# Performance work log

Measured on AMD Instinct MI355X. Metric: run time of the kernel, lower is better.

The kernel has to match this reference:

```python
import math
import jax, jax.numpy as jnp
import numpy as np

B, CIN, COUT, K, T, S = 16, 512, 512, 3, 2048, 128


def setup_inputs() -> dict:
    key = jax.random.key(0)
    k1, k2, k3, k4 = jax.random.split(key, 4)
    x = jax.random.normal(k1, (B, CIN, T), dtype=jnp.float32)
    c_trg = jax.random.normal(k2, (B, S), dtype=jnp.float32)
    style_w = jax.random.normal(k3, (CIN, S), dtype=jnp.float32)  # EqualLinear weight (lr_mul=1)
    style_b = jnp.ones((CIN,), dtype=jnp.float32)  # bias_init=1
    conv_w = jax.random.normal(k4, (1, COUT, CIN, K), dtype=jnp.float32)
    return {"x": x, "c_trg": c_trg, "style_w": style_w, "style_b": style_b, "conv_w": conv_w}


def reference(x, c_trg, style_w, style_b, conv_w):
    b, cin, t = x.shape
    cout, k = conv_w.shape[1], conv_w.shape[3]
    lin_scale = 1.0 / math.sqrt(style_w.shape[1])  # EqualLinear scale, lr_mul=1
    # original forward calls style_linear twice -> s and b are the SAME value
    s = c_trg @ (style_w * lin_scale).T + style_b            # [B, Cin]
    s = s[:, None, :, None]                                   # [B, 1, Cin, 1]
    conv_scale = 1.0 / math.sqrt(cin * k ** 2)
    w = conv_scale * (conv_w * s + s)                         # [B, Cout, Cin, K]
    demod = jax.lax.rsqrt(jnp.sum(w * w, axis=(2, 3)) + 1e-8)  # [B, Cout]
    demod_mean = jnp.mean(w.reshape(b, cout, -1), axis=2)      # [B, Cout]
    w = (w - demod_mean[:, :, None, None]) * demod[:, :, None, None]
    pad = k // 2

    def conv1(xi, wi):  # xi [Cin, T], wi [Cout, Cin, K]
        return jax.lax.conv_general_dilated(
            xi[None], wi, window_strides=(1,), padding=[(pad, pad)],
            dimension_numbers=("NCH", "OIH", "NCH"))[0]

    out = jax.vmap(conv1)(x, w)  # [B, Cout, T]
    return out
```

## Files before the change

### kernel.cpp

```cpp
#include <hip/hip_runtime.h>
#include <hip/hip_bf16.h>
#include <stdint.h>

#define B_    16
#define CIN_  512
#define COUT_ 512
#define K_    3
#define T_    2048
#define S_    128
#define TP_   2064
#define CXP_  2050

#define LIN_SCALE  0.08838834764831845f
#define CONV_SCALE 0.014731391274719739f

typedef unsigned short u16;
typedef short s16x8 __attribute__((ext_vector_type(8)));
typedef float f32x4 __attribute__((ext_vector_type(4)));
typedef u16 u16x8 __attribute__((ext_vector_type(8)));

__device__ __forceinline__ u16 bf16r(float f) {
    uint32_t u = __float_as_uint(f);
    return (u16)((u + 0x7FFFu + ((u >> 16) & 1u)) >> 16);
}

#define GLDS16(gsrc, ldst) \
    __builtin_amdgcn_global_load_lds((__attribute__((address_space(1))) void*)(gsrc), \
                                     (__attribute__((address_space(3))) void*)(ldst), 16, 0, 0)

__global__ void k_style(const float* __restrict__ c_trg,
                        const float* __restrict__ style_w,
                        const float* __restrict__ style_b,
                        float* __restrict__ s_out) {
    int idx = blockIdx.x * 256 + threadIdx.x;
    int b = idx >> 9, i = idx & 511;
    const float4* c4 = reinterpret_cast<const float4*>(c_trg + b * S_);
    const float4* w4 = reinterpret_cast<const float4*>(style_w + (size_t)i * S_);
    float acc = 0.f;
#pragma unroll
    for (int j = 0; j < S_ / 4; ++j) {
        float4 a = c4[j], w = w4[j];
        acc += a.x * w.x + a.y * w.y + a.z * w.z + a.w * w.w;
    }
    s_out[idx] = acc * LIN_SCALE + style_b[i];
}

__global__ void k_wsum(const float* __restrict__ conv_w,
                       float* __restrict__ W1, float* __restrict__ W2) {
    int idx = blockIdx.x * 256 + threadIdx.x;
    const float* wr = conv_w + (size_t)idx * 3;
    float a0 = wr[0] + 1.f, a1 = wr[1] + 1.f, a2 = wr[2] + 1.f;
    W1[idx] = a0 + a1 + a2;
    W2[idx] = a0 * a0 + a1 * a1 + a2 * a2;
}

__global__ void k_stats2(const float* __restrict__ s,
                         const float* __restrict__ W1, const float* __restrict__ W2,
                         float* __restrict__ alpha, float* __restrict__ beta) {
    int bo = blockIdx.x;
    int b = bo >> 9, o = bo & 511;
    const float* sb = s + b * CIN_;
    const float* w1 = W1 + (size_t)o * CIN_;
    const float* w2 = W2 + (size_t)o * CIN_;
    int l = threadIdx.x;
    float sum = 0.f, sq = 0.f;
#pragma unroll
    for (int r = 0; r < 8; ++r) {
        float sv = sb[l + r * 64];
        sum += sv * w1[l + r * 64];
        sq  += sv * sv * w2[l + r * 64];
    }
#pragma unroll
    for (int off = 32; off; off >>= 1) { sum += __shfl_down(sum, off); sq += __shfl_down(sq, off); }
    if (l == 0) {
        float mean  = CONV_SCALE * sum * (1.0f / (CIN_ * K_));
        float demod = rsqrtf(CONV_SCALE * CONV_SCALE * sq + 1e-8f);
        alpha[bo] = demod * CONV_SCALE;
        beta[bo]  = demod * mean;
    }
}

__global__ void k_prep_w(const float* __restrict__ conv_w, u16* __restrict__ wpk) {
    int idx = blockIdx.x * 256 + threadIdx.x;
    int j    = idx & 7;
    int lane = (idx >> 3) & 63;
    int grp  = (idx >> 9) & 7;
    int rest = idx >> 12;
    int tap  = rest % 3;
    int so   = rest / 3;
    int step = so & 15, ob = so >> 4;
    int o = ob * 128 + grp * 16 + (lane & 15);
    int i = step * 32 + (lane >> 4) * 8 + j;
    wpk[idx] = bf16r(conv_w[((size_t)o * CIN_ + i) * 3 + tap]);
}

__global__ void k_ytrans(const float* __restrict__ x, const float* __restrict__ s,
                         u16* __restrict__ ybf,
                         float* __restrict__ cxp, float* __restrict__ cyp) {
    int t = blockIdx.x * 256 + threadIdx.x;
    int oct = blockIdx.y, b = blockIdx.z;
    const float* xb = x + ((size_t)(b * CIN_ + oct * 8)) * T_ + t;
    const float* sb = s + b * CIN_ + oct * 8;
    float ax = 0.f, ay = 0.f;
    u16x8 pv;
#pragma unroll
    for (int j = 0; j < 8; ++j) {
        float xv = xb[(size_t)j * T_];
        float yv = sb[j] * xv;
        ax += xv; ay += yv;
        pv[j] = bf16r(yv);
    }
    *(u16x8*)(ybf + (((size_t)(b * 64 + oct)) * TP_ + t + 8) * 8) = pv;
    atomicAdd(&cxp[b * CXP_ + t + 1], ax);
    atomicAdd(&cyp[b * CXP_ + t + 1], ay);
    if (blockIdx.x == 0 && threadIdx.x < 8) {
        u16x8 z = {0, 0, 0, 0, 0, 0, 0, 0};
        *(u16x8*)(ybf + (((size_t)(b * 64 + oct)) * TP_ + threadIdx.x) * 8) = z;
    }
    if (blockIdx.x == 7 && threadIdx.x >= 248) {
        u16x8 z = {0, 0, 0, 0, 0, 0, 0, 0};
        *(u16x8*)(ybf + (((size_t)(b * 64 + oct)) * TP_ + 2056 + (threadIdx.x - 248)) * 8) = z;
    }
}

__global__ __launch_bounds__(256) void k_conv(
    const u16* __restrict__ wpk, const u16* __restrict__ ybf,
    const float* __restrict__ alpha, const float* __restrict__ beta,
    const float* __restrict__ cxp, const float* __restrict__ cyp,
    float* __restrict__ out) {

    __shared__ __align__(16) char smem[33792];

    const int tid  = threadIdx.x;
    const int lane = tid & 63;
    const int w    = tid >> 6;
    const int wr   = w >> 1, wc = w & 1;
    const int t0   = blockIdx.x * 128;
    const int ob   = blockIdx.y;
    const int b    = blockIdx.z;

    f32x4 acc[4][4] = {};

    const char* wsrc  = (const char*)wpk + (size_t)(ob * 16) * 24576 + (w * 6) * 1024 + lane * 16;
    const char* ybase = (const char*)ybf + ((size_t)b * 64) * (TP_ * 16);

    const int as_lane = wr * 4096 + lane * 16;
    const int xs_lane = 24576 + (lane >> 4) * 2304 + ((lane & 15) + 7) * 16 + wc * 1024;

    for (int step = 0; step < 16; ++step) {
        __syncthreads();
#pragma unroll
        for (int r = 0; r < 6; ++r)
            GLDS16(wsrc + (size_t)step * 24576 + r * 1024, smem + (w * 6 + r) * 1024);
#pragma unroll
        for (int rb = w; rb < 9; rb += 4) {
            int c  = rb * 64 + lane;
            int g  = c / 144;
            int rr = c - g * 144;
            GLDS16(ybase + ((size_t)((step * 4 + g) * TP_) + t0 + rr) * 16,
                   smem + 24576 + rb * 1024);
        }
        __syncthreads();

#pragma unroll
        for (int tap = 0; tap < 3; ++tap) {
            s16x8 af[4], bq[4];
#pragma unroll
            for (int m = 0; m < 4; ++m)
                af[m] = *(const s16x8*)(smem + tap * 8192 + as_lane + m * 1024);
#pragma unroll
            for (int n = 0; n < 4; ++n)
                bq[n] = *(const s16x8*)(smem + xs_lane + tap * 16 + n * 256);
#pragma unroll
            for (int m = 0; m < 4; ++m)
#pragma unroll
                for (int n = 0; n < 4; ++n)
                    acc[m][n] = __builtin_amdgcn_mfma_f32_16x16x32_bf16(af[m], bq[n], acc[m][n], 0, 0, 0);
        }
    }

    const int lr = lane >> 4, lc = lane & 15;
    const int o0 = ob * 128 + wr * 64;
    const int tw = t0 + wc * 64;
    const float* al  = alpha + b * COUT_ + o0;
    const float* be  = beta  + b * COUT_ + o0;
    const float* cxb = cxp + b * CXP_;
    const float* cyb = cyp + b * CXP_;
    float* op = out + ((size_t)(b * COUT_ + o0)) * T_;

#pragma unroll
    for (int n = 0; n < 4; ++n) {
        int t = tw + n * 16 + lc;
        float cx3 = cxb[t] + cxb[t + 1] + cxb[t + 2];
        float cy3 = cyb[t] + cyb[t + 1] + cyb[t + 2];
#pragma unroll
        for (int m = 0; m < 4; ++m)
#pragma unroll
            for (int q = 0; q < 4; ++q) {
                int o = m * 16 + lr * 4 + q;
                op[(size_t)o * T_ + t] = al[o] * (acc[m][n][q] + cy3) - be[o] * cx3;
            }
    }
}

extern "C" void kernel_launch(void* const* d_in, const int* in_sizes, int n_in,
                              void* d_out, int out_size, void* d_ws, size_t ws_size,
                              hipStream_t stream) {
    const float* x       = (const float*)d_in[0];
    const float* c_trg   = (const float*)d_in[1];
    const float* style_w = (const float*)d_in[2];
    const float* style_b = (const float*)d_in[3];
    const float* conv_w  = (const float*)d_in[4];
    float* out = (float*)d_out;
    float* ws  = (float*)d_ws;

    float* s_buf = ws;
    float* alpha = ws + 8192;
    float* beta  = ws + 16384;
    float* cxp   = ws + 24576;
    float* cyp   = ws + 57376;
    float* W1    = ws + 90176;
    float* W2    = ws + 352320;
    u16*   wpk   = (u16*)(ws + 614464);
    u16*   ybf   = (u16*)(ws + 1007680);

    hipMemsetAsync(cxp, 0, (size_t)2 * CXP_ * B_ * sizeof(float), stream);

    k_style <<<dim3((B_ * CIN_) / 256), 256, 0, stream>>>(c_trg, style_w, style_b, s_buf);
    k_wsum  <<<dim3((COUT_ * CIN_) / 256), 256, 0, stream>>>(conv_w, W1, W2);
    k_prep_w<<<dim3((COUT_ * CIN_ * K_) / 256), 256, 0, stream>>>(conv_w, wpk);
    k_stats2<<<dim3(B_ * COUT_), 64, 0, stream>>>(s_buf, W1, W2, alpha, beta);
    k_ytrans<<<dim3(T_ / 256, CIN_ / 8, B_), 256, 0, stream>>>(x, s_buf, ybf, cxp, cyp);
    k_conv  <<<dim3(T_ / 128, COUT_ / 128, B_), 256, 0, stream>>>(wpk, ybf, alpha, beta, cxp, cyp, out);
}
```

Before: 226.2 us.

## Double-buffer conv LDS loads, remap blocks, replace atomic column sums with reduction

```diff
diff --git a/kernel.cpp b/kernel.cpp
--- a/kernel.cpp
+++ b/kernel.cpp
@@ -96,7 +96,7 @@
 
 __global__ void k_ytrans(const float* __restrict__ x, const float* __restrict__ s,
                          u16* __restrict__ ybf,
-                         float* __restrict__ cxp, float* __restrict__ cyp) {
+                         float* __restrict__ cxpart, float* __restrict__ cypart) {
     int t = blockIdx.x * 256 + threadIdx.x;
     int oct = blockIdx.y, b = blockIdx.z;
     const float* xb = x + ((size_t)(b * CIN_ + oct * 8)) * T_ + t;
@@ -111,8 +111,8 @@
         pv[j] = bf16r(yv);
     }
     *(u16x8*)(ybf + (((size_t)(b * 64 + oct)) * TP_ + t + 8) * 8) = pv;
-    atomicAdd(&cxp[b * CXP_ + t + 1], ax);
-    atomicAdd(&cyp[b * CXP_ + t + 1], ay);
+    cxpart[((size_t)(b * 64 + oct)) * T_ + t] = ax;
+    cypart[((size_t)(b * 64 + oct)) * T_ + t] = ay;
     if (blockIdx.x == 0 && threadIdx.x < 8) {
         u16x8 z = {0, 0, 0, 0, 0, 0, 0, 0};
         *(u16x8*)(ybf + (((size_t)(b * 64 + oct)) * TP_ + threadIdx.x) * 8) = z;
@@ -121,6 +121,22 @@
         u16x8 z = {0, 0, 0, 0, 0, 0, 0, 0};
         *(u16x8*)(ybf + (((size_t)(b * 64 + oct)) * TP_ + 2056 + (threadIdx.x - 248)) * 8) = z;
     }
+}
+
+__global__ void k_colred(const float* __restrict__ cxpart, const float* __restrict__ cypart,
+                         float* __restrict__ cxp, float* __restrict__ cyp) {
+    int t = blockIdx.x * 256 + threadIdx.x;
+    int b = blockIdx.y;
+    float sx = 0.f, sy = 0.f;
+#pragma unroll 8
+    for (int oct = 0; oct < 64; ++oct) {
+        sx += cxpart[((size_t)(b * 64 + oct)) * T_ + t];
+        sy += cypart[((size_t)(b * 64 + oct)) * T_ + t];
+    }
+    cxp[b * CXP_ + t + 1] = sx;
+    cyp[b * CXP_ + t + 1] = sy;
+    if (t == 0)        { cxp[b * CXP_] = 0.f;        cyp[b * CXP_] = 0.f; }
+    if (t == T_ - 1)   { cxp[b * CXP_ + T_ + 1] = 0.f; cyp[b * CXP_ + T_ + 1] = 0.f; }
 }
 
 __global__ __launch_bounds__(256) void k_conv(
@@ -129,15 +145,18 @@
     const float* __restrict__ cxp, const float* __restrict__ cyp,
     float* __restrict__ out) {
 
-    __shared__ __align__(16) char smem[33792];
+    __shared__ __align__(16) char smem[2 * 33792];
 
     const int tid  = threadIdx.x;
     const int lane = tid & 63;
     const int w    = tid >> 6;
     const int wr   = w >> 1, wc = w & 1;
-    const int t0   = blockIdx.x * 128;
-    const int ob   = blockIdx.y;
-    const int b    = blockIdx.z;
+
+    const int bid = blockIdx.x;
+    const int wg  = (bid & 7) * 128 + (bid >> 3);
+    const int b   = wg >> 6;
+    const int ob  = (wg >> 4) & 3;
+    const int t0  = (wg & 15) * 128;
 
     f32x4 acc[4][4] = {};
 
@@ -147,37 +166,49 @@
     const int as_lane = wr * 4096 + lane * 16;
     const int xs_lane = 24576 + (lane >> 4) * 2304 + ((lane & 15) + 7) * 16 + wc * 1024;
 
+#define STAGE(buf, step)                                                              \
+    do {                                                                              \
+        char* dst = smem + (buf) * 33792;                                             \
+        _Pragma("unroll")                                                             \
+        for (int r = 0; r < 6; ++r)                                                   \
+            GLDS16(wsrc + (size_t)(step) * 24576 + r * 1024, dst + (w * 6 + r) * 1024); \
+        _Pragma("unroll")                                                             \
+        for (int rb = w; rb < 9; rb += 4) {                                           \
+            int c  = rb * 64 + lane;                                                  \
+            int g  = c / 144;                                                         \
+            int rr = c - g * 144;                                                     \
+            GLDS16(ybase + ((size_t)(((step) * 4 + g) * TP_) + t0 + rr) * 16,         \
+                   dst + 24576 + rb * 1024);                                          \
+        }                                                                             \
+    } while (0)
+
+    STAGE(0, 0);
+    __syncthreads();
+
+    int cur = 0;
     for (int step = 0; step < 16; ++step) {
-        __syncthreads();
-#pragma unroll
-        for (int r = 0; r < 6; ++r)
-            GLDS16(wsrc + (size_t)step * 24576 + r * 1024, smem + (w * 6 + r) * 1024);
-#pragma unroll
-        for (int rb = w; rb < 9; rb += 4) {
-            int c  = rb * 64 + lane;
-            int g  = c / 144;
-            int rr = c - g * 144;
-            GLDS16(ybase + ((size_t)((step * 4 + g) * TP_) + t0 + rr) * 16,
-                   smem + 24576 + rb * 1024);
-        }
-        __syncthreads();
-
+        if (step < 15) STAGE(cur ^ 1, step + 1);
+
+        const char* base = smem + cur * 33792;
 #pragma unroll
         for (int tap = 0; tap < 3; ++tap) {
             s16x8 af[4], bq[4];
 #pragma unroll
             for (int m = 0; m < 4; ++m)
-                af[m] = *(const s16x8*)(smem + tap * 8192 + as_lane + m * 1024);
+                af[m] = *(const s16x8*)(base + tap * 8192 + as_lane + m * 1024);
 #pragma unroll
             for (int n = 0; n < 4; ++n)
-                bq[n] = *(const s16x8*)(smem + xs_lane + tap * 16 + n * 256);
+                bq[n] = *(const s16x8*)(base + xs_lane + tap * 16 + n * 256);
 #pragma unroll
             for (int m = 0; m < 4; ++m)
 #pragma unroll
                 for (int n = 0; n < 4; ++n)
                     acc[m][n] = __builtin_amdgcn_mfma_f32_16x16x32_bf16(af[m], bq[n], acc[m][n], 0, 0, 0);
         }
-    }
+        __syncthreads();
+        cur ^= 1;
+    }
+#undef STAGE
 
     const int lr = lane >> 4, lc = lane & 15;
     const int o0 = ob * 128 + wr * 64;
@@ -224,12 +255,14 @@
     u16*   wpk   = (u16*)(ws + 614464);
     u16*   ybf   = (u16*)(ws + 1007680);
 
-    hipMemsetAsync(cxp, 0, (size_t)2 * CXP_ * B_ * sizeof(float), stream);
+    float* cxpart = out;
+    float* cypart = out + (size_t)B_ * 64 * T_;
 
     k_style <<<dim3((B_ * CIN_) / 256), 256, 0, stream>>>(c_trg, style_w, style_b, s_buf);
     k_wsum  <<<dim3((COUT_ * CIN_) / 256), 256, 0, stream>>>(conv_w, W1, W2);
     k_prep_w<<<dim3((COUT_ * CIN_ * K_) / 256), 256, 0, stream>>>(conv_w, wpk);
     k_stats2<<<dim3(B_ * COUT_), 64, 0, stream>>>(s_buf, W1, W2, alpha, beta);
-    k_ytrans<<<dim3(T_ / 256, CIN_ / 8, B_), 256, 0, stream>>>(x, s_buf, ybf, cxp, cyp);
-    k_conv  <<<dim3(T_ / 128, COUT_ / 128, B_), 256, 0, stream>>>(wpk, ybf, alpha, beta, cxp, cyp, out);
-}
+    k_ytrans<<<dim3(T_ / 256, CIN_ / 8, B_), 256, 0, stream>>>(x, s_buf, ybf, cxpart, cypart);
+    k_colred<<<dim3(T_ / 256, B_), 256, 0, stream>>>(cxpart, cypart, cxp, cyp);
+    k_conv  <<<dim3(1024), 256, 0, stream>>>(wpk, ybf, alpha, beta, cxp, cyp, out);
+}
```

Result: faster. 190.7 us (-15.7%).

## Pipeline conv with triple-buffered LDS, register-loaded weights, larger tiles, swizzled grid

Applied to the files above, without the earlier changes.

```diff
diff --git a/kernel.cpp b/kernel.cpp
--- a/kernel.cpp
+++ b/kernel.cpp
@@ -10,6 +10,8 @@
 #define S_    128
 #define TP_   2064
 #define CXP_  2050
+#define XS_SZ 17408
+#define NBUF  3
 
 #define LIN_SCALE  0.08838834764831845f
 #define CONV_SCALE 0.014731391274719739f
@@ -97,87 +99,122 @@
 __global__ void k_ytrans(const float* __restrict__ x, const float* __restrict__ s,
                          u16* __restrict__ ybf,
                          float* __restrict__ cxp, float* __restrict__ cyp) {
-    int t = blockIdx.x * 256 + threadIdx.x;
-    int oct = blockIdx.y, b = blockIdx.z;
-    const float* xb = x + ((size_t)(b * CIN_ + oct * 8)) * T_ + t;
-    const float* sb = s + b * CIN_ + oct * 8;
+    int tid = threadIdx.x;
+    int t = blockIdx.x * 256 + tid;
+    int og = blockIdx.y, b = blockIdx.z;
     float ax = 0.f, ay = 0.f;
-    u16x8 pv;
-#pragma unroll
-    for (int j = 0; j < 8; ++j) {
-        float xv = xb[(size_t)j * T_];
-        float yv = sb[j] * xv;
-        ax += xv; ay += yv;
-        pv[j] = bf16r(yv);
-    }
-    *(u16x8*)(ybf + (((size_t)(b * 64 + oct)) * TP_ + t + 8) * 8) = pv;
+#pragma unroll
+    for (int o8 = 0; o8 < 8; ++o8) {
+        int oct = og * 8 + o8;
+        const float* xb = x + ((size_t)(b * CIN_ + oct * 8)) * T_ + t;
+        const float* sb = s + b * CIN_ + oct * 8;
+        u16x8 pv;
+#pragma unroll
+        for (int j = 0; j < 8; ++j) {
+            float xv = xb[(size_t)j * T_];
+            float yv = sb[j] * xv;
+            ax += xv; ay += yv;
+            pv[j] = bf16r(yv);
+        }
+        *(u16x8*)(ybf + (((size_t)(b * 64 + oct)) * TP_ + t + 8) * 8) = pv;
+    }
     atomicAdd(&cxp[b * CXP_ + t + 1], ax);
     atomicAdd(&cyp[b * CXP_ + t + 1], ay);
-    if (blockIdx.x == 0 && threadIdx.x < 8) {
+    if (blockIdx.x == 0 && tid < 64) {
         u16x8 z = {0, 0, 0, 0, 0, 0, 0, 0};
-        *(u16x8*)(ybf + (((size_t)(b * 64 + oct)) * TP_ + threadIdx.x) * 8) = z;
-    }
-    if (blockIdx.x == 7 && threadIdx.x >= 248) {
-        u16x8 z = {0, 0, 0, 0, 0, 0, 0, 0};
-        *(u16x8*)(ybf + (((size_t)(b * 64 + oct)) * TP_ + 2056 + (threadIdx.x - 248)) * 8) = z;
-    }
-}
-
-__global__ __launch_bounds__(256) void k_conv(
+        int oct = og * 8 + (tid >> 3);
+        *(u16x8*)(ybf + (((size_t)(b * 64 + oct)) * TP_ + (tid & 7)) * 8) = z;
+        *(u16x8*)(ybf + (((size_t)(b * 64 + oct)) * TP_ + 2056 + (tid & 7)) * 8) = z;
+    }
+}
+
+__global__ __launch_bounds__(512) void k_conv(
     const u16* __restrict__ wpk, const u16* __restrict__ ybf,
     const float* __restrict__ alpha, const float* __restrict__ beta,
     const float* __restrict__ cxp, const float* __restrict__ cyp,
     float* __restrict__ out) {
 
-    __shared__ __align__(16) char smem[33792];
+    __shared__ __align__(16) char smem[NBUF * XS_SZ];
 
     const int tid  = threadIdx.x;
     const int lane = tid & 63;
     const int w    = tid >> 6;
-    const int wr   = w >> 1, wc = w & 1;
-    const int t0   = blockIdx.x * 128;
-    const int ob   = blockIdx.y;
-    const int b    = blockIdx.z;
+    const int wr   = w >> 2, wc = w & 3;
+
+    const int bid = blockIdx.x;
+    const int wg  = (bid & 7) * 64 + (bid >> 3);
+    const int b   = wg >> 5;
+    const int ob  = (wg >> 3) & 3;
+    const int t0  = (wg & 7) * 256;
+
+    const int row0 = tid, row1 = 512 + tid, row2 = 1024 + w * 8 + (lane & 7);
+    const int g0 = row0 / 272, rr0 = row0 - g0 * 272;
+    const int g1 = row1 / 272, rr1 = row1 - g1 * 272;
+    const int g2 = row2 / 272, rr2 = row2 - g2 * 272;
+
+    const char* ybase = (const char*)ybf + ((size_t)b * 64) * (TP_ * 16);
+    const char* abase = (const char*)wpk + (size_t)ob * 393216 + (wr * 4) * 1024 + lane * 16;
+    const int xs_lane = (lane >> 4) * 4352 + ((lane & 15) + 7) * 16 + wc * 1024;
 
     f32x4 acc[4][4] = {};
-
-    const char* wsrc  = (const char*)wpk + (size_t)(ob * 16) * 24576 + (w * 6) * 1024 + lane * 16;
-    const char* ybase = (const char*)ybf + ((size_t)b * 64) * (TP_ * 16);
-
-    const int as_lane = wr * 4096 + lane * 16;
-    const int xs_lane = 24576 + (lane >> 4) * 2304 + ((lane & 15) + 7) * 16 + wc * 1024;
-
-    for (int step = 0; step < 16; ++step) {
-        __syncthreads();
-#pragma unroll
-        for (int r = 0; r < 6; ++r)
-            GLDS16(wsrc + (size_t)step * 24576 + r * 1024, smem + (w * 6 + r) * 1024);
-#pragma unroll
-        for (int rb = w; rb < 9; rb += 4) {
-            int c  = rb * 64 + lane;
-            int g  = c / 144;
-            int rr = c - g * 144;
-            GLDS16(ybase + ((size_t)((step * 4 + g) * TP_) + t0 + rr) * 16,
-                   smem + 24576 + rb * 1024);
-        }
-        __syncthreads();
-
-#pragma unroll
-        for (int tap = 0; tap < 3; ++tap) {
-            s16x8 af[4], bq[4];
-#pragma unroll
-            for (int m = 0; m < 4; ++m)
-                af[m] = *(const s16x8*)(smem + tap * 8192 + as_lane + m * 1024);
-#pragma unroll
-            for (int n = 0; n < 4; ++n)
-                bq[n] = *(const s16x8*)(smem + xs_lane + tap * 16 + n * 256);
-#pragma unroll
-            for (int m = 0; m < 4; ++m)
-#pragma unroll
-                for (int n = 0; n < 4; ++n)
-                    acc[m][n] = __builtin_amdgcn_mfma_f32_16x16x32_bf16(af[m], bq[n], acc[m][n], 0, 0, 0);
-        }
-    }
+    s16x8 afA[12], afB[12];
+
+#define STAGEB(s)                                                                        \
+    do {                                                                                 \
+        char* bb = smem + ((s) % NBUF) * XS_SZ;                                          \
+        GLDS16(ybase + ((size_t)(((s) * 4 + g0) * TP_) + t0 + rr0) * 16, bb + row0 * 16); \
+        GLDS16(ybase + ((size_t)(((s) * 4 + g1) * TP_) + t0 + rr1) * 16, bb + row1 * 16); \
+        if ((tid & 63) < 8)                                                              \
+            GLDS16(ybase + ((size_t)(((s) * 4 + g2) * TP_) + t0 + rr2) * 16, bb + row2 * 16); \
+    } while (0)
+
+#define LOADA(dst, s)                                                                    \
+    do {                                                                                 \
+        _Pragma("unroll")                                                                \
+        for (int u = 0; u < 12; ++u)                                                     \
+            dst[u] = *(const s16x8*)(abase + (size_t)(s) * 24576 + (u >> 2) * 8192 + (u & 3) * 1024); \
+    } while (0)
+
+#define BODY(s, CUR, NXT)                                                                \
+    do {                                                                                 \
+        asm volatile("" ::: "memory");                                                   \
+        __builtin_amdgcn_s_barrier();                                                    \
+        asm volatile("" ::: "memory");                                                   \
+        __builtin_amdgcn_sched_barrier(0);                                               \
+        if ((s) <= 13) STAGEB((s) + 2);                                                  \
+        if ((s) <= 14) LOADA(NXT, (s) + 1);                                              \
+        {                                                                                \
+            const char* bbuf = smem + ((s) % NBUF) * XS_SZ;                              \
+            __builtin_amdgcn_s_setprio(1);                                               \
+            _Pragma("unroll")                                                            \
+            for (int tap = 0; tap < 3; ++tap) {                                          \
+                s16x8 bq[4];                                                             \
+                _Pragma("unroll")                                                        \
+                for (int n = 0; n < 4; ++n)                                              \
+                    bq[n] = *(const s16x8*)(bbuf + xs_lane + tap * 16 + n * 256);        \
+                _Pragma("unroll")                                                        \
+                for (int m = 0; m < 4; ++m)                                              \
+                    _Pragma("unroll")                                                    \
+                    for (int n = 0; n < 4; ++n)                                          \
+                        acc[m][n] = __builtin_amdgcn_mfma_f32_16x16x32_bf16(             \
+                            CUR[tap * 4 + m], bq[n], acc[m][n], 0, 0, 0);                \
+            }                                                                            \
+            __builtin_amdgcn_s_setprio(0);                                               \
+        }                                                                                \
+    } while (0)
+
+    STAGEB(0);
+    STAGEB(1);
+    LOADA(afA, 0);
+
+    for (int it = 0; it < 8; ++it) {
+        const int s0 = it * 2;
+        BODY(s0, afA, afB);
+        BODY(s0 + 1, afB, afA);
+    }
+#undef BODY
+#undef LOADA
+#undef STAGEB
 
     const int lr = lane >> 4, lc = lane & 15;
     const int o0 = ob * 128 + wr * 64;
@@ -230,6 +267,6 @@
     k_wsum  <<<dim3((COUT_ * CIN_) / 256), 256, 0, stream>>>(conv_w, W1, W2);
     k_prep_w<<<dim3((COUT_ * CIN_ * K_) / 256), 256, 0, stream>>>(conv_w, wpk);
     k_stats2<<<dim3(B_ * COUT_), 64, 0, stream>>>(s_buf, W1, W2, alpha, beta);
-    k_ytrans<<<dim3(T_ / 256, CIN_ / 8, B_), 256, 0, stream>>>(x, s_buf, ybf, cxp, cyp);
-    k_conv  <<<dim3(T_ / 128, COUT_ / 128, B_), 256, 0, stream>>>(wpk, ybf, alpha, beta, cxp, cyp, out);
-}
+    k_ytrans<<<dim3(T_ / 256, 8, B_), 256, 0, stream>>>(x, s_buf, ybf, cxp, cyp);
+    k_conv  <<<dim3(512), 512, 0, stream>>>(wpk, ybf, alpha, beta, cxp, cyp, out);
+}
```

Result: faster. 192.3 us (-15.0%).
